# Kernel optimization log

Measured on AMD Instinct MI355X. Metric: run time of the kernel, lower is better.

Reference implementation:

```python
import jax, jax.numpy as jnp
import numpy as np

B, SRC_LEN, IN_DIM = 4096, 128, 16
H = 64
SEQ_LEN = 100
MEAN_DIM = 4
COV_DIM = MEAN_DIM + MEAN_DIM * (MEAN_DIM - 1) // 2  # 10
SKIP = 4


def _lin_init(key, out_d, in_d):
    k1, k2 = jax.random.split(key)
    bound = 1.0 / np.sqrt(in_d)
    W = jax.random.uniform(k1, (out_d, in_d), minval=-bound, maxval=bound, dtype=jnp.float32)
    b = jax.random.uniform(k2, (out_d,), minval=-bound, maxval=bound, dtype=jnp.float32)
    return W, b


def setup_inputs() -> dict:
    key = jax.random.key(0)
    ks = jax.random.split(key, 16)
    inp = {}
    inp["x"] = jax.random.normal(ks[0], (B, SRC_LEN, IN_DIM), dtype=jnp.float32)
    inp["trg"] = jax.random.normal(ks[1], (B, 1, SKIP), dtype=jnp.float32)
    # encoder GRU (1 layer)
    inp["enc_Wih"], inp["enc_bih"] = _lin_init(ks[2], 3 * H, IN_DIM)
    inp["enc_Whh"], inp["enc_bhh"] = _lin_init(ks[3], 3 * H, H)
    # decoder GRU (1 layer)
    inp["dec_Wih"], inp["dec_bih"] = _lin_init(ks[4], 3 * H, IN_DIM)
    inp["dec_Whh"], inp["dec_bhh"] = _lin_init(ks[5], 3 * H, H)
    # decoder.out: Linear(H -> IN_DIM)
    inp["out_W"], inp["out_b"] = _lin_init(ks[6], IN_DIM, H)
    # initEmbed: Linear(SKIP -> IN_DIM)
    inp["emb_W"], inp["emb_b"] = _lin_init(ks[7], IN_DIM, SKIP)
    # mean head: Linear(IN_DIM->H), GELU, Linear(H->MEAN_DIM)
    inp["mh_W1"], inp["mh_b1"] = _lin_init(ks[8], H, IN_DIM)
    inp["mh_W2"], inp["mh_b2"] = _lin_init(ks[9], MEAN_DIM, H)
    # cov head: Linear(IN_DIM->H), GELU, Linear(H->COV_DIM)
    inp["ch_W1"], inp["ch_b1"] = _lin_init(ks[10], H, IN_DIM)
    inp["ch_W2"], inp["ch_b2"] = _lin_init(ks[11], COV_DIM, H)
    return inp


def _gru_cell(h, xt, Wih, Whh, bih, bhh):
    # PyTorch GRU cell math. h, xt: [B, H], [B, in]
    gi = xt @ Wih.T + bih           # [B, 3H]
    gh = h @ Whh.T + bhh            # [B, 3H]
    i_r, i_z, i_n = jnp.split(gi, 3, axis=-1)
    h_r, h_z, h_n = jnp.split(gh, 3, axis=-1)
    r = jax.nn.sigmoid(i_r + h_r)
    z = jax.nn.sigmoid(i_z + h_z)
    n = jnp.tanh(i_n + r * h_n)
    return (1.0 - z) * n + z * h


def reference(x, trg, enc_Wih, enc_bih, enc_Whh, enc_bhh,
              dec_Wih, dec_bih, dec_Whh, dec_bhh,
              out_W, out_b, emb_W, emb_b,
              mh_W1, mh_b1, mh_W2, mh_b2,
              ch_W1, ch_b1, ch_W2, ch_b2):
    b = x.shape[0]
    # ---- encoder GRU over src_len; only final hidden is used downstream ----
    h0 = jnp.zeros((b, H), dtype=x.dtype)

    def enc_step(h, xt):
        h = _gru_cell(h, xt, enc_Wih, enc_Whh, enc_bih, enc_bhh)
        return h, None

    enc_h, _ = jax.lax.scan(enc_step, h0, jnp.swapaxes(x, 0, 1))

    init_in = trg[:, 0, :] @ emb_W.T + emb_b  # [B, IN_DIM]

    def dec_step(carry, _):
        h, inp = carry
        h = _gru_cell(h, inp, dec_Wih, dec_Whh, dec_bih, dec_bhh)
        o = h @ out_W.T + out_b               # [B, IN_DIM]
        nxt = jax.lax.stop_gradient(o)        # .detach() on fed-back input
        return (h, nxt), o

    (_, _), outs = jax.lax.scan(dec_step, (enc_h, init_in), None, length=SEQ_LEN)
    dec_out = jnp.swapaxes(outs, 0, 1)        # [B, SEQ_LEN, IN_DIM]

    # ---- output heads (Dropout is identity in eval) ----
    means = jax.nn.gelu(dec_out @ mh_W1.T + mh_b1, approximate=False) @ mh_W2.T + mh_b2
    covs = jax.nn.gelu(dec_out @ ch_W1.T + ch_b1, approximate=False) @ ch_W2.T + ch_b2

    inf = jnp.inf
    lower = jnp.array([-inf, -inf, -1.0, -1.0], dtype=means.dtype)
    upper = jnp.array([inf, inf, 1.0, 1.0], dtype=means.dtype)
    means = jnp.maximum(jnp.minimum(means, upper), lower)
    return means, covs
```

## Files before the change

### kernel.cpp

```cpp
#include <hip/hip_runtime.h>
#include <cstdint>
#include <cstddef>

#define BTOT    4096
#define SRCLEN  128
#define INDIM   16
#define HDIM    64
#define SEQLEN  100
#define MEANS_N (BTOT * SEQLEN * 4)

__device__ __forceinline__ float sigmoidf_(float x) {
    return __builtin_amdgcn_rcpf(1.0f + __expf(-x));
}
__device__ __forceinline__ float tanhf_(float x) {
    float e = __expf(2.0f * x);
    return 1.0f - 2.0f * __builtin_amdgcn_rcpf(e + 1.0f);
}
__device__ __forceinline__ float gelu_fast(float x) {
    float z = fabsf(x) * 0.70710678118654752440f;
    float t = __builtin_amdgcn_rcpf(1.0f + 0.3275911f * z);
    float p = t * (0.254829592f +
              t * (-0.284496736f +
              t * (1.421413741f +
              t * (-1.453152027f +
              t * 1.061405429f))));
    float er = 1.0f - p * __expf(-z * z);
    er = copysignf(er, x);
    return 0.5f * x * (1.0f + er);
}

typedef __attribute__((ext_vector_type(8))) short s8v;
typedef __attribute__((ext_vector_type(4))) float f4v;

__device__ __forceinline__ unsigned short f2bf(float x) {
    unsigned u = __float_as_uint(x);
    unsigned r = (u + 0x7FFFu + ((u >> 16) & 1u)) >> 16;
    return (unsigned short)r;
}
__device__ __forceinline__ float bf2f(unsigned short b) {
    return __uint_as_float(((unsigned)b) << 16);
}
__device__ __forceinline__ void split2(float4 a, float4 b, s8v& hi, s8v& lo) {
    float v[8] = {a.x, a.y, a.z, a.w, b.x, b.y, b.z, b.w};
    #pragma unroll
    for (int j = 0; j < 8; ++j) {
        unsigned short h = f2bf(v[j]);
        hi[j] = (short)h;
        lo[j] = (short)f2bf(v[j] - bf2f(h));
    }
}
__device__ __forceinline__ void split8(const float* v, s8v& hi, s8v& lo) {
    #pragma unroll
    for (int j = 0; j < 8; ++j) {
        unsigned short h = f2bf(v[j]);
        hi[j] = (short)h;
        lo[j] = (short)f2bf(v[j] - bf2f(h));
    }
}
__device__ __forceinline__ void load_bfrag(const float* p, s8v& hi, s8v& lo) {
    float4 a = *(const float4*)p;
    float4 b = *(const float4*)(p + 4);
    split2(a, b, hi, lo);
}

typedef __attribute__((ext_vector_type(2))) unsigned int u2v;
__device__ __forceinline__ float half_merge(float own_lo, float send_hi) {
    u2v r = __builtin_amdgcn_permlane32_swap(__float_as_uint(own_lo),
                                             __float_as_uint(send_hi),
                                             false, false);
    return __uint_as_float(r[0]);
}

#define MFMA16(a, b, c) __builtin_amdgcn_mfma_f32_16x16x32_bf16((a), (b), (c), 0, 0, 0)

__global__ __launch_bounds__(256, 2) void fused_gru_kernel(
    const float* __restrict__ x,
    const float* __restrict__ eWih, const float* __restrict__ ebih,
    const float* __restrict__ eWhh, const float* __restrict__ ebhh,
    const float* __restrict__ dWih, const float* __restrict__ dbih,
    const float* __restrict__ dWhh, const float* __restrict__ dbhh,
    const float* __restrict__ outW, const float* __restrict__ outb,
    const float* __restrict__ embW, const float* __restrict__ embb,
    const float* __restrict__ trg,
    float* __restrict__ dec_o)
{
    const int tid  = threadIdx.x;
    const int lane = tid & 63;
    const int w    = tid >> 6;
    const int col  = lane & 15;
    const int q    = lane >> 4;
    const int u    = w * 16 + col;
    const int b0   = blockIdx.x * 8;
    const int rj0  = (q & 1) * 4 + ((q >> 1) << 1);

    __shared__ __align__(16) unsigned short hiL[2][16][72];
    __shared__ __align__(16) unsigned short loL[2][16][72];
    __shared__ __align__(16) unsigned short xhi_l[64][9][16];
    __shared__ __align__(16) unsigned short xlo_l[64][9][16];
    __shared__ float outW_l[16][64];
    __shared__ float init_l[8][16];

    for (int i = tid; i < 16 * 64; i += 256) outW_l[i >> 6][i & 63] = outW[i];
    if (tid < 128) {
        int b = tid >> 4, jj = tid & 15;
        float s = embb[jj];
        #pragma unroll
        for (int s4 = 0; s4 < 4; ++s4)
            s = fmaf(embW[jj * 4 + s4], trg[(size_t)(b0 + b) * 4 + s4], s);
        init_l[b][jj] = s;
    }

    for (int i = tid; i < 2 * 16 * 72; i += 256) {
        ((unsigned short*)hiL)[i] = 0;
        ((unsigned short*)loL)[i] = 0;
    }
    for (int i = tid; i < 64 * 16; i += 256) {
        xhi_l[i >> 4][8][i & 15] = 0;
        xlo_l[i >> 4][8][i & 15] = 0;
    }

    auto stage_x = [&](int c) {
        #pragma unroll
        for (int k = 0; k < 8; ++k) {
            int f   = tid + k * 256;
            int b   = f >> 8;
            int rem = f & 255;
            int tl  = rem >> 2;
            int d4  = (rem & 3) << 2;
            const float* xp = x + ((size_t)(b0 + b) * SRCLEN + (c * 64 + tl)) * INDIM + d4;
            float4 v = *(const float4*)xp;
            float vv[4] = {v.x, v.y, v.z, v.w};
            unsigned short hh[4], ll[4];
            #pragma unroll
            for (int j = 0; j < 4; ++j) {
                hh[j] = f2bf(vv[j]);
                ll[j] = f2bf(vv[j] - bf2f(hh[j]));
            }
            *(ushort4*)&xhi_l[tl][b][d4] = make_ushort4(hh[0], hh[1], hh[2], hh[3]);
            *(ushort4*)&xlo_l[tl][b][d4] = make_ushort4(ll[0], ll[1], ll[2], ll[3]);
        }
    };

    const s8v z8 = {0, 0, 0, 0, 0, 0, 0, 0};
    const f4v z4 = {0.0f, 0.0f, 0.0f, 0.0f};

    {
        s8v brh[3], brl[3], bzh[3], bzl[3], bnhh[2], bnhl[2], bnxh, bnxl;
        load_bfrag(eWhh + (size_t)u * 64 + q * 8,              brh[0], brl[0]);
        load_bfrag(eWhh + (size_t)u * 64 + 32 + q * 8,         brh[1], brl[1]);
        load_bfrag(eWhh + (size_t)(64 + u) * 64 + q * 8,       bzh[0], bzl[0]);
        load_bfrag(eWhh + (size_t)(64 + u) * 64 + 32 + q * 8,  bzh[1], bzl[1]);
        load_bfrag(eWhh + (size_t)(128 + u) * 64 + q * 8,      bnhh[0], bnhl[0]);
        load_bfrag(eWhh + (size_t)(128 + u) * 64 + 32 + q * 8, bnhh[1], bnhl[1]);
        if (q < 2) {
            load_bfrag(eWih + (size_t)u * 16 + q * 8,         brh[2], brl[2]);
            load_bfrag(eWih + (size_t)(64 + u) * 16 + q * 8,  bzh[2], bzl[2]);
            load_bfrag(eWih + (size_t)(128 + u) * 16 + q * 8, bnxh, bnxl);
        } else {
            brh[2] = z8; brl[2] = z8; bzh[2] = z8; bzl[2] = z8; bnxh = z8; bnxl = z8;
        }

        const float br   = ebih[u] + ebhh[u];
        const float bz   = ebih[u + 64] + ebhh[u + 64];
        const float bnx  = ebih[u + 128];
        const float bnh  = ebhh[u + 128];

        const int xb   = (q < 2) ? (col & 7) : 8;
        const int xoff = (q & 1) * 8;
        const unsigned short* xh_base = &xhi_l[0][xb][xoff];
        const unsigned short* xl_base = &xlo_l[0][xb][xoff];

        stage_x(0);
        float hold2e[2] = {0.0f, 0.0f};
        __syncthreads();

        int cur = 0;
        for (int t = 0; t < SRCLEN; ++t) {
            if (t == 64) {
                stage_x(1);
                __syncthreads();
            }
            const int tl = t & 63;

            const s8v xh = *(const s8v*)(xh_base + (size_t)tl * 144);
            const s8v xl = *(const s8v*)(xl_base + (size_t)tl * 144);

            const s8v ah0 = *(const s8v*)&hiL[cur][col][q * 8];
            const s8v al0 = *(const s8v*)&loL[cur][col][q * 8];
            const s8v ah1 = *(const s8v*)&hiL[cur][col][32 + q * 8];
            const s8v al1 = *(const s8v*)&loL[cur][col][32 + q * 8];

            f4v accr, accz, accnh, accnx;
            accr  = MFMA16(ah0, brh[0], z4);
            accz  = MFMA16(ah0, bzh[0], z4);
            accnh = MFMA16(ah0, bnhh[0], z4);
            accr  = MFMA16(ah0, brl[0], accr);
            accz  = MFMA16(ah0, bzl[0], accz);
            accnh = MFMA16(ah0, bnhl[0], accnh);
            accr  = MFMA16(al0, brh[0], accr);
            accz  = MFMA16(al0, bzh[0], accz);
            accnh = MFMA16(al0, bnhh[0], accnh);
            accr  = MFMA16(ah1, brh[1], accr);
            accz  = MFMA16(ah1, bzh[1], accz);
            accnh = MFMA16(ah1, bnhh[1], accnh);
            accr  = MFMA16(ah1, brl[1], accr);
            accz  = MFMA16(ah1, bzl[1], accz);
            accnh = MFMA16(ah1, bnhl[1], accnh);
            accr  = MFMA16(al1, brh[1], accr);
            accz  = MFMA16(al1, bzh[1], accz);
            accnh = MFMA16(al1, bnhh[1], accnh);
            accr  = MFMA16(xh, brh[2], accr);
            accz  = MFMA16(xh, bzh[2], accz);
            accnx = MFMA16(xh, bnxh, z4);
            accr  = MFMA16(xh, brl[2], accr);
            accz  = MFMA16(xh, bzl[2], accz);
            accnx = MFMA16(xh, bnxl, accnx);
            accr  = MFMA16(xl, brh[2], accr);
            accz  = MFMA16(xl, bzh[2], accz);
            accnx = MFMA16(xl, bnxh, accnx);

            float pr[2], pz[2], pnh[2], pnx[2];
            pr[0]  = half_merge(accr[0],  accr[2]);
            pr[1]  = half_merge(accr[1],  accr[3]);
            pz[0]  = half_merge(accz[0],  accz[2]);
            pz[1]  = half_merge(accz[1],  accz[3]);
            pnh[0] = half_merge(accnh[0], accnh[2]);
            pnh[1] = half_merge(accnh[1], accnh[3]);
            pnx[0] = half_merge(accnx[0], accnx[2]);
            pnx[1] = half_merge(accnx[1], accnx[3]);

            const int nxt = cur ^ 1;
            #pragma unroll
            for (int j = 0; j < 2; ++j) {
                float r  = sigmoidf_(pr[j] + br);
                float zz = sigmoidf_(pz[j] + bz);
                float n  = tanhf_(pnx[j] + bnx + r * (pnh[j] + bnh));
                float h  = (1.0f - zz) * n + zz * hold2e[j];
                hold2e[j] = h;
                unsigned short hh = f2bf(h);
                hiL[nxt][rj0 + j][u] = hh;
                loL[nxt][rj0 + j][u] = f2bf(h - bf2f(hh));
            }
            __syncthreads();
            cur ^= 1;
        }

        float hold2[2] = {hold2e[0], hold2e[1]};

        float wh_r[16], wh_z[16], wh_n[16];
        #pragma unroll
        for (int c = 0; c < 2; ++c)
            #pragma unroll
            for (int jj = 0; jj < 8; ++jj) {
                int k = c * 32 + q * 8 + jj;
                wh_r[c * 8 + jj] = dWhh[(size_t)u * 64 + k];
                wh_z[c * 8 + jj] = dWhh[(size_t)(64 + u) * 64 + k];
                wh_n[c * 8 + jj] = dWhh[(size_t)(128 + u) * 64 + k];
            }
        float wi_r[16], wi_z[16], wi_n[16];
        #pragma unroll
        for (int j = 0; j < 16; ++j) {
            wi_r[j] = dWih[(size_t)u * 16 + j];
            wi_z[j] = dWih[(size_t)(64 + u) * 16 + j];
            wi_n[j] = dWih[(size_t)(128 + u) * 16 + j];
        }

        float m_r[16], m_z[16], c_in[16];
        #pragma unroll
        for (int c = 0; c < 2; ++c)
            #pragma unroll
            for (int jj = 0; jj < 8; ++jj) {
                int k = c * 32 + q * 8 + jj;
                float sr = 0.0f, sz = 0.0f, sn = 0.0f;
                #pragma unroll
                for (int j = 0; j < 16; ++j) {
                    float ow = outW_l[j][k];
                    sr = fmaf(wi_r[j], ow, sr);
                    sz = fmaf(wi_z[j], ow, sz);
                    sn = fmaf(wi_n[j], ow, sn);
                }
                m_r[c * 8 + jj]  = wh_r[c * 8 + jj] + sr;
                m_z[c * 8 + jj]  = wh_z[c * 8 + jj] + sz;
                c_in[c * 8 + jj] = sn;
            }

        s8v mrh[2], mrl[2], mzh[2], mzl[2], cinh[2], cinl[2], hnh[2], hnl[2];
        split8(m_r,      mrh[0],  mrl[0]);  split8(m_r + 8,  mrh[1],  mrl[1]);
        split8(m_z,      mzh[0],  mzl[0]);  split8(m_z + 8,  mzh[1],  mzl[1]);
        split8(c_in,     cinh[0], cinl[0]); split8(c_in + 8, cinh[1], cinl[1]);
        split8(wh_n,     hnh[0],  hnl[0]);  split8(wh_n + 8, hnh[1],  hnl[1]);
        s8v r0h[2], r0l[2], z0h[2], z0l[2];
        split8(wh_r, r0h[0], r0l[0]); split8(wh_r + 8, r0h[1], r0l[1]);
        split8(wh_z, z0h[0], z0l[0]); split8(wh_z + 8, z0h[1], z0l[1]);
        s8v owh[2], owl[2];
        {
            float ov[16];
            #pragma unroll
            for (int c = 0; c < 2; ++c)
                #pragma unroll
                for (int jj = 0; jj < 8; ++jj)
                    ov[c * 8 + jj] = outW_l[col][c * 32 + q * 8 + jj];
            split8(ov, owh[0], owl[0]); split8(ov + 8, owh[1], owl[1]);
        }

        float b_r = dbhh[u] + dbih[u];
        float b_z = dbhh[u + 64] + dbih[u + 64];
        float b_in = dbih[u + 128];
        const float b_hn = dbhh[u + 128];
        #pragma unroll
        for (int j = 0; j < 16; ++j) {
            float obj = outb[j];
            b_r  = fmaf(obj, wi_r[j], b_r);
            b_z  = fmaf(obj, wi_z[j], b_z);
            b_in = fmaf(obj, wi_n[j], b_in);
        }
        const float ob = outb[col];

        float g_r[2], g_z[2], g_n[2];
        #pragma unroll
        for (int j2 = 0; j2 < 2; ++j2) {
            int row = rj0 + j2;
            float sr = dbih[u] + dbhh[u];
            float sz = dbih[u + 64] + dbhh[u + 64];
            float sn = dbih[u + 128];
            #pragma unroll
            for (int j = 0; j < 16; ++j) {
                float iv = init_l[row][j];
                sr = fmaf(wi_r[j], iv, sr);
                sz = fmaf(wi_z[j], iv, sz);
                sn = fmaf(wi_n[j], iv, sn);
            }
            g_r[j2] = sr; g_z[j2] = sz; g_n[j2] = sn;
        }

        {
            const s8v ah0 = *(const s8v*)&hiL[0][col][q * 8];
            const s8v al0 = *(const s8v*)&loL[0][col][q * 8];
            const s8v ah1 = *(const s8v*)&hiL[0][col][32 + q * 8];
            const s8v al1 = *(const s8v*)&loL[0][col][32 + q * 8];
            f4v ar, az, ahn;
            ar  = MFMA16(ah0, r0h[0], z4);
            az  = MFMA16(ah0, z0h[0], z4);
            ahn = MFMA16(ah0, hnh[0], z4);
            ar  = MFMA16(ah0, r0l[0], ar);
            az  = MFMA16(ah0, z0l[0], az);
            ahn = MFMA16(ah0, hnl[0], ahn);
            ar  = MFMA16(al0, r0h[0], ar);
            az  = MFMA16(al0, z0h[0], az);
            ahn = MFMA16(al0, hnh[0], ahn);
            ar  = MFMA16(ah1, r0h[1], ar);
            az  = MFMA16(ah1, z0h[1], az);
            ahn = MFMA16(ah1, hnh[1], ahn);
            ar  = MFMA16(ah1, r0l[1], ar);
            az  = MFMA16(ah1, z0l[1], az);
            ahn = MFMA16(ah1, hnl[1], ahn);
            ar  = MFMA16(al1, r0h[1], ar);
            az  = MFMA16(al1, z0h[1], az);
            ahn = MFMA16(al1, hnh[1], ahn);

            float pr[2], pz[2], pnh[2];
            pr[0]  = half_merge(ar[0],  ar[2]);
            pr[1]  = half_merge(ar[1],  ar[3]);
            pz[0]  = half_merge(az[0],  az[2]);
            pz[1]  = half_merge(az[1],  az[3]);
            pnh[0] = half_merge(ahn[0], ahn[2]);
            pnh[1] = half_merge(ahn[1], ahn[3]);

            #pragma unroll
            for (int j = 0; j < 2; ++j) {
                float r  = sigmoidf_(pr[j] + g_r[j]);
                float zz = sigmoidf_(pz[j] + g_z[j]);
                float n  = tanhf_(g_n[j] + r * (pnh[j] + b_hn));
                float h  = (1.0f - zz) * n + zz * hold2[j];
                hold2[j] = h;
                unsigned short hh = f2bf(h);
                hiL[1][rj0 + j][u] = hh;
                loL[1][rj0 + j][u] = f2bf(h - bf2f(hh));
            }
            __syncthreads();
        }

        for (int t = 1; t < SEQLEN; ++t) {
            const int dcur = t & 1;
            const s8v ah0 = *(const s8v*)&hiL[dcur][col][q * 8];
            const s8v al0 = *(const s8v*)&loL[dcur][col][q * 8];
            const s8v ah1 = *(const s8v*)&hiL[dcur][col][32 + q * 8];
            const s8v al1 = *(const s8v*)&loL[dcur][col][32 + q * 8];

            if (w == ((t - 1) & 3)) {
                f4v oa;
                oa = MFMA16(ah0, owh[0], z4);
                oa = MFMA16(ah0, owl[0], oa);
                oa = MFMA16(al0, owh[0], oa);
                oa = MFMA16(ah1, owh[1], oa);
                oa = MFMA16(ah1, owl[1], oa);
                oa = MFMA16(al1, owh[1], oa);
                if (q < 2) {
                    #pragma unroll
                    for (int i = 0; i < 4; ++i)
                        dec_o[(((size_t)(b0 + q * 4 + i) * SEQLEN) + (t - 1)) * INDIM + col] = oa[i] + ob;
                }
            }

            f4v ar, az, ain, ahn;
            ar  = MFMA16(ah0, mrh[0], z4);
            az  = MFMA16(ah0, mzh[0], z4);
            ain = MFMA16(ah0, cinh[0], z4);
            ahn = MFMA16(ah0, hnh[0], z4);
            ar  = MFMA16(ah0, mrl[0], ar);
            az  = MFMA16(ah0, mzl[0], az);
            ain = MFMA16(ah0, cinl[0], ain);
            ahn = MFMA16(ah0, hnl[0], ahn);
            ar  = MFMA16(al0, mrh[0], ar);
            az  = MFMA16(al0, mzh[0], az);
            ain = MFMA16(al0, cinh[0], ain);
            ahn = MFMA16(al0, hnh[0], ahn);
            ar  = MFMA16(ah1, mrh[1], ar);
            az  = MFMA16(ah1, mzh[1], az);
            ain = MFMA16(ah1, cinh[1], ain);
            ahn = MFMA16(ah1, hnh[1], ahn);
            ar  = MFMA16(ah1, mrl[1], ar);
            az  = MFMA16(ah1, mzl[1], az);
            ain = MFMA16(ah1, cinl[1], ain);
            ahn = MFMA16(ah1, hnl[1], ahn);
            ar  = MFMA16(al1, mrh[1], ar);
            az  = MFMA16(al1, mzh[1], az);
            ain = MFMA16(al1, cinh[1], ain);
            ahn = MFMA16(al1, hnh[1], ahn);

            float pr[2], pz[2], pin[2], pnh[2];
            pr[0]  = half_merge(ar[0],  ar[2]);
            pr[1]  = half_merge(ar[1],  ar[3]);
            pz[0]  = half_merge(az[0],  az[2]);
            pz[1]  = half_merge(az[1],  az[3]);
            pin[0] = half_merge(ain[0], ain[2]);
            pin[1] = half_merge(ain[1], ain[3]);
            pnh[0] = half_merge(ahn[0], ahn[2]);
            pnh[1] = half_merge(ahn[1], ahn[3]);

            const int nxt = dcur ^ 1;
            #pragma unroll
            for (int j = 0; j < 2; ++j) {
                float r  = sigmoidf_(pr[j] + b_r);
                float zz = sigmoidf_(pz[j] + b_z);
                float n  = tanhf_(pin[j] + b_in + r * (pnh[j] + b_hn));
                float h  = (1.0f - zz) * n + zz * hold2[j];
                hold2[j] = h;
                unsigned short hh = f2bf(h);
                hiL[nxt][rj0 + j][u] = hh;
                loL[nxt][rj0 + j][u] = f2bf(h - bf2f(hh));
            }
            __syncthreads();
        }

        if (w == 0) {
            const s8v ah0 = *(const s8v*)&hiL[0][col][q * 8];
            const s8v al0 = *(const s8v*)&loL[0][col][q * 8];
            const s8v ah1 = *(const s8v*)&hiL[0][col][32 + q * 8];
            const s8v al1 = *(const s8v*)&loL[0][col][32 + q * 8];
            f4v oa;
            oa = MFMA16(ah0, owh[0], z4);
            oa = MFMA16(ah0, owl[0], oa);
            oa = MFMA16(al0, owh[0], oa);
            oa = MFMA16(ah1, owh[1], oa);
            oa = MFMA16(ah1, owl[1], oa);
            oa = MFMA16(al1, owh[1], oa);
            if (q < 2) {
                #pragma unroll
                for (int i = 0; i < 4; ++i)
                    dec_o[(((size_t)(b0 + q * 4 + i) * SEQLEN) + (SEQLEN - 1)) * INDIM + col] = oa[i] + ob;
            }
        }
    }
}

__global__ __launch_bounds__(256) void heads_kernel(
    const float* __restrict__ dec_o,
    const float* __restrict__ mW1, const float* __restrict__ mb1,
    const float* __restrict__ mW2, const float* __restrict__ mb2,
    const float* __restrict__ cW1, const float* __restrict__ cb1,
    const float* __restrict__ cW2, const float* __restrict__ cb2,
    float* __restrict__ out)
{
    const int tid = threadIdx.x;

    __shared__ __align__(16) float lW1m[64][16];
    __shared__ __align__(16) float lW1c[64][16];
    __shared__ __align__(16) float lW2t[64][16];

    for (int i = tid; i < 1024; i += 256) {
        lW1m[i >> 4][i & 15] = mW1[i];
        lW1c[i >> 4][i & 15] = cW1[i];
    }
    if (tid < 64) {
        #pragma unroll
        for (int j = 0; j < 4; ++j)  lW2t[tid][j]     = mW2[j * 64 + tid];
        #pragma unroll
        for (int j = 0; j < 10; ++j) lW2t[tid][4 + j] = cW2[j * 64 + tid];
        lW2t[tid][14] = mb1[tid];
        lW2t[tid][15] = cb1[tid];
    }
    __syncthreads();

    const size_t r0 = (size_t)blockIdx.x * 512 + tid;

    float o[2][16];
    #pragma unroll
    for (int k = 0; k < 2; ++k) {
        const float4* op = (const float4*)(dec_o + (r0 + (size_t)k * 256) * 16);
        #pragma unroll
        for (int c = 0; c < 4; ++c) {
            float4 v = op[c];
            o[k][4 * c + 0] = v.x; o[k][4 * c + 1] = v.y;
            o[k][4 * c + 2] = v.z; o[k][4 * c + 3] = v.w;
        }
    }

    float m[2][4], cv[2][10];
    #pragma unroll
    for (int k = 0; k < 2; ++k) {
        #pragma unroll
        for (int j = 0; j < 4; ++j)  m[k][j]  = mb2[j];
        #pragma unroll
        for (int j = 0; j < 10; ++j) cv[k][j] = cb2[j];
    }

    #pragma unroll 2
    for (int hu = 0; hu < 64; ++hu) {
        const float4 a0 = *(const float4*)&lW1m[hu][0];
        const float4 a1 = *(const float4*)&lW1m[hu][4];
        const float4 a2 = *(const float4*)&lW1m[hu][8];
        const float4 a3 = *(const float4*)&lW1m[hu][12];
        const float4 c0 = *(const float4*)&lW1c[hu][0];
        const float4 c1 = *(const float4*)&lW1c[hu][4];
        const float4 c2 = *(const float4*)&lW1c[hu][8];
        const float4 c3 = *(const float4*)&lW1c[hu][12];
        const float4 t0 = *(const float4*)&lW2t[hu][0];
        const float4 t1 = *(const float4*)&lW2t[hu][4];
        const float4 t2 = *(const float4*)&lW2t[hu][8];
        const float4 t3 = *(const float4*)&lW2t[hu][12];

        #pragma unroll
        for (int k = 0; k < 2; ++k) {
            float hm = t3.z;
            hm = fmaf(a0.x, o[k][0],  hm); hm = fmaf(a0.y, o[k][1],  hm);
            hm = fmaf(a0.z, o[k][2],  hm); hm = fmaf(a0.w, o[k][3],  hm);
            hm = fmaf(a1.x, o[k][4],  hm); hm = fmaf(a1.y, o[k][5],  hm);
            hm = fmaf(a1.z, o[k][6],  hm); hm = fmaf(a1.w, o[k][7],  hm);
            hm = fmaf(a2.x, o[k][8],  hm); hm = fmaf(a2.y, o[k][9],  hm);
            hm = fmaf(a2.z, o[k][10], hm); hm = fmaf(a2.w, o[k][11], hm);
            hm = fmaf(a3.x, o[k][12], hm); hm = fmaf(a3.y, o[k][13], hm);
            hm = fmaf(a3.z, o[k][14], hm); hm = fmaf(a3.w, o[k][15], hm);
            float gm = gelu_fast(hm);
            m[k][0] = fmaf(t0.x, gm, m[k][0]); m[k][1] = fmaf(t0.y, gm, m[k][1]);
            m[k][2] = fmaf(t0.z, gm, m[k][2]); m[k][3] = fmaf(t0.w, gm, m[k][3]);

            float hc = t3.w;
            hc = fmaf(c0.x, o[k][0],  hc); hc = fmaf(c0.y, o[k][1],  hc);
            hc = fmaf(c0.z, o[k][2],  hc); hc = fmaf(c0.w, o[k][3],  hc);
            hc = fmaf(c1.x, o[k][4],  hc); hc = fmaf(c1.y, o[k][5],  hc);
            hc = fmaf(c1.z, o[k][6],  hc); hc = fmaf(c1.w, o[k][7],  hc);
            hc = fmaf(c2.x, o[k][8],  hc); hc = fmaf(c2.y, o[k][9],  hc);
            hc = fmaf(c2.z, o[k][10], hc); hc = fmaf(c2.w, o[k][11], hc);
            hc = fmaf(c3.x, o[k][12], hc); hc = fmaf(c3.y, o[k][13], hc);
            hc = fmaf(c3.z, o[k][14], hc); hc = fmaf(c3.w, o[k][15], hc);
            float gc = gelu_fast(hc);
            cv[k][0] = fmaf(t1.x, gc, cv[k][0]); cv[k][1] = fmaf(t1.y, gc, cv[k][1]);
            cv[k][2] = fmaf(t1.z, gc, cv[k][2]); cv[k][3] = fmaf(t1.w, gc, cv[k][3]);
            cv[k][4] = fmaf(t2.x, gc, cv[k][4]); cv[k][5] = fmaf(t2.y, gc, cv[k][5]);
            cv[k][6] = fmaf(t2.z, gc, cv[k][6]); cv[k][7] = fmaf(t2.w, gc, cv[k][7]);
            cv[k][8] = fmaf(t3.x, gc, cv[k][8]); cv[k][9] = fmaf(t3.y, gc, cv[k][9]);
        }
    }

    float* means = out;
    float* covs  = out + MEANS_N;
    #pragma unroll
    for (int k = 0; k < 2; ++k) {
        const size_t r = r0 + (size_t)k * 256;
        m[k][2] = fminf(fmaxf(m[k][2], -1.0f), 1.0f);
        m[k][3] = fminf(fmaxf(m[k][3], -1.0f), 1.0f);
        #pragma unroll
        for (int j = 0; j < 4; ++j)  means[r * 4 + j] = m[k][j];
        #pragma unroll
        for (int j = 0; j < 10; ++j) covs[r * 10 + j] = cv[k][j];
    }
}

extern "C" void kernel_launch(void* const* d_in, const int* in_sizes, int n_in,
                              void* d_out, int out_size, void* d_ws, size_t ws_size,
                              hipStream_t stream)
{
    const float* x    = (const float*)d_in[0];
    const float* trg  = (const float*)d_in[1];
    const float* eWih = (const float*)d_in[2];
    const float* ebih = (const float*)d_in[3];
    const float* eWhh = (const float*)d_in[4];
    const float* ebhh = (const float*)d_in[5];
    const float* dWih = (const float*)d_in[6];
    const float* dbih = (const float*)d_in[7];
    const float* dWhh = (const float*)d_in[8];
    const float* dbhh = (const float*)d_in[9];
    const float* outW = (const float*)d_in[10];
    const float* outb = (const float*)d_in[11];
    const float* embW = (const float*)d_in[12];
    const float* embb = (const float*)d_in[13];
    const float* mW1  = (const float*)d_in[14];
    const float* mb1  = (const float*)d_in[15];
    const float* mW2  = (const float*)d_in[16];
    const float* mb2  = (const float*)d_in[17];
    const float* cW1  = (const float*)d_in[18];
    const float* cb1  = (const float*)d_in[19];
    const float* cW2  = (const float*)d_in[20];
    const float* cb2  = (const float*)d_in[21];

    float* ws    = (float*)d_ws;
    float* dec_o = ws;
    float* outp  = (float*)d_out;

    fused_gru_kernel<<<dim3(BTOT / 8), dim3(256), 0, stream>>>(
        x, eWih, ebih, eWhh, ebhh, dWih, dbih, dWhh, dbhh,
        outW, outb, embW, embb, trg, dec_o);
    heads_kernel<<<dim3((BTOT * SEQLEN) / 512), dim3(256), 0, stream>>>(
        dec_o, mW1, mb1, mW2, mb2, cW1, cb1, cW2, cb2, outp);
}
```

Measured before the change: 358.4 us.

## Rewrite output heads kernel with split-bf16 MFMA matmuls

Replaces the scalar FMA head MLP with a per-wave MFMA formulation. Both linear layers of the mean and cov heads use bf16 hi/lo split products (three MFMAs per product) to keep near-fp32 accuracy. The GELU hidden activations are staged through LDS as bf16 hi/lo pairs. Each wave handles four 16-row tiles. This aims to cut the VALU-bound FMA cost of the heads, but adds LDS traffic and stores only partially utilized MFMA output columns.

```diff
diff --git a/kernel.cpp b/kernel.cpp
--- a/kernel.cpp
+++ b/kernel.cpp
@@ -474,7 +474,7 @@
     }
 }
 
-__global__ __launch_bounds__(256) void heads_kernel(
+__global__ __launch_bounds__(256) void heads_mfma_kernel(
     const float* __restrict__ dec_o,
     const float* __restrict__ mW1, const float* __restrict__ mb1,
     const float* __restrict__ mW2, const float* __restrict__ mb2,
@@ -482,108 +482,125 @@
     const float* __restrict__ cW2, const float* __restrict__ cb2,
     float* __restrict__ out)
 {
-    const int tid = threadIdx.x;
-
-    __shared__ __align__(16) float lW1m[64][16];
-    __shared__ __align__(16) float lW1c[64][16];
-    __shared__ __align__(16) float lW2t[64][16];
-
-    for (int i = tid; i < 1024; i += 256) {
-        lW1m[i >> 4][i & 15] = mW1[i];
-        lW1c[i >> 4][i & 15] = cW1[i];
-    }
-    if (tid < 64) {
-        #pragma unroll
-        for (int j = 0; j < 4; ++j)  lW2t[tid][j]     = mW2[j * 64 + tid];
-        #pragma unroll
-        for (int j = 0; j < 10; ++j) lW2t[tid][4 + j] = cW2[j * 64 + tid];
-        lW2t[tid][14] = mb1[tid];
-        lW2t[tid][15] = cb1[tid];
-    }
-    __syncthreads();
-
-    const size_t r0 = (size_t)blockIdx.x * 512 + tid;
-
-    float o[2][16];
+    const int tid  = threadIdx.x;
+    const int lane = tid & 63;
+    const int w    = tid >> 6;
+    const int col  = lane & 15;
+    const int q    = lane >> 4;
+
+    __shared__ __align__(16) unsigned short Hm_hi[4][16][72];
+    __shared__ __align__(16) unsigned short Hm_lo[4][16][72];
+    __shared__ __align__(16) unsigned short Hc_hi[4][16][72];
+    __shared__ __align__(16) unsigned short Hc_lo[4][16][72];
+
+    const s8v z8 = {0, 0, 0, 0, 0, 0, 0, 0};
+    const f4v z4 = {0.0f, 0.0f, 0.0f, 0.0f};
+
+    s8v w1mh[4], w1ml[4], w1ch[4], w1cl[4];
     #pragma unroll
-    for (int k = 0; k < 2; ++k) {
-        const float4* op = (const float4*)(dec_o + (r0 + (size_t)k * 256) * 16);
-        #pragma unroll
-        for (int c = 0; c < 4; ++c) {
-            float4 v = op[c];
-            o[k][4 * c + 0] = v.x; o[k][4 * c + 1] = v.y;
-            o[k][4 * c + 2] = v.z; o[k][4 * c + 3] = v.w;
-        }
-    }
-
-    float m[2][4], cv[2][10];
+    for (int c = 0; c < 4; ++c) {
+        if (q < 2) {
+            load_bfrag(mW1 + (size_t)(c * 16 + col) * 16 + q * 8, w1mh[c], w1ml[c]);
+            load_bfrag(cW1 + (size_t)(c * 16 + col) * 16 + q * 8, w1ch[c], w1cl[c]);
+        } else {
+            w1mh[c] = z8; w1ml[c] = z8; w1ch[c] = z8; w1cl[c] = z8;
+        }
+    }
+    s8v w2mh[2], w2ml[2], w2ch[2], w2cl[2];
+    if (col < 4) {
+        load_bfrag(mW2 + (size_t)col * 64 + q * 8,      w2mh[0], w2ml[0]);
+        load_bfrag(mW2 + (size_t)col * 64 + 32 + q * 8, w2mh[1], w2ml[1]);
+    } else {
+        w2mh[0] = z8; w2ml[0] = z8; w2mh[1] = z8; w2ml[1] = z8;
+    }
+    if (col < 10) {
+        load_bfrag(cW2 + (size_t)col * 64 + q * 8,      w2ch[0], w2cl[0]);
+        load_bfrag(cW2 + (size_t)col * 64 + 32 + q * 8, w2ch[1], w2cl[1]);
+    } else {
+        w2ch[0] = z8; w2cl[0] = z8; w2ch[1] = z8; w2cl[1] = z8;
+    }
+
+    float b1m[4], b1c[4];
     #pragma unroll
-    for (int k = 0; k < 2; ++k) {
-        #pragma unroll
-        for (int j = 0; j < 4; ++j)  m[k][j]  = mb2[j];
-        #pragma unroll
-        for (int j = 0; j < 10; ++j) cv[k][j] = cb2[j];
-    }
-
-    #pragma unroll 2
-    for (int hu = 0; hu < 64; ++hu) {
-        const float4 a0 = *(const float4*)&lW1m[hu][0];
-        const float4 a1 = *(const float4*)&lW1m[hu][4];
-        const float4 a2 = *(const float4*)&lW1m[hu][8];
-        const float4 a3 = *(const float4*)&lW1m[hu][12];
-        const float4 c0 = *(const float4*)&lW1c[hu][0];
-        const float4 c1 = *(const float4*)&lW1c[hu][4];
-        const float4 c2 = *(const float4*)&lW1c[hu][8];
-        const float4 c3 = *(const float4*)&lW1c[hu][12];
-        const float4 t0 = *(const float4*)&lW2t[hu][0];
-        const float4 t1 = *(const float4*)&lW2t[hu][4];
-        const float4 t2 = *(const float4*)&lW2t[hu][8];
-        const float4 t3 = *(const float4*)&lW2t[hu][12];
-
-        #pragma unroll
-        for (int k = 0; k < 2; ++k) {
-            float hm = t3.z;
-            hm = fmaf(a0.x, o[k][0],  hm); hm = fmaf(a0.y, o[k][1],  hm);
-            hm = fmaf(a0.z, o[k][2],  hm); hm = fmaf(a0.w, o[k][3],  hm);
-            hm = fmaf(a1.x, o[k][4],  hm); hm = fmaf(a1.y, o[k][5],  hm);
-            hm = fmaf(a1.z, o[k][6],  hm); hm = fmaf(a1.w, o[k][7],  hm);
-            hm = fmaf(a2.x, o[k][8],  hm); hm = fmaf(a2.y, o[k][9],  hm);
-            hm = fmaf(a2.z, o[k][10], hm); hm = fmaf(a2.w, o[k][11], hm);
-            hm = fmaf(a3.x, o[k][12], hm); hm = fmaf(a3.y, o[k][13], hm);
-            hm = fmaf(a3.z, o[k][14], hm); hm = fmaf(a3.w, o[k][15], hm);
-            float gm = gelu_fast(hm);
-            m[k][0] = fmaf(t0.x, gm, m[k][0]); m[k][1] = fmaf(t0.y, gm, m[k][1]);
-            m[k][2] = fmaf(t0.z, gm, m[k][2]); m[k][3] = fmaf(t0.w, gm, m[k][3]);
-
-            float hc = t3.w;
-            hc = fmaf(c0.x, o[k][0],  hc); hc = fmaf(c0.y, o[k][1],  hc);
-            hc = fmaf(c0.z, o[k][2],  hc); hc = fmaf(c0.w, o[k][3],  hc);
-            hc = fmaf(c1.x, o[k][4],  hc); hc = fmaf(c1.y, o[k][5],  hc);
-            hc = fmaf(c1.z, o[k][6],  hc); hc = fmaf(c1.w, o[k][7],  hc);
-            hc = fmaf(c2.x, o[k][8],  hc); hc = fmaf(c2.y, o[k][9],  hc);
-            hc = fmaf(c2.z, o[k][10], hc); hc = fmaf(c2.w, o[k][11], hc);
-            hc = fmaf(c3.x, o[k][12], hc); hc = fmaf(c3.y, o[k][13], hc);
-            hc = fmaf(c3.z, o[k][14], hc); hc = fmaf(c3.w, o[k][15], hc);
-            float gc = gelu_fast(hc);
-            cv[k][0] = fmaf(t1.x, gc, cv[k][0]); cv[k][1] = fmaf(t1.y, gc, cv[k][1]);
-            cv[k][2] = fmaf(t1.z, gc, cv[k][2]); cv[k][3] = fmaf(t1.w, gc, cv[k][3]);
-            cv[k][4] = fmaf(t2.x, gc, cv[k][4]); cv[k][5] = fmaf(t2.y, gc, cv[k][5]);
-            cv[k][6] = fmaf(t2.z, gc, cv[k][6]); cv[k][7] = fmaf(t2.w, gc, cv[k][7]);
-            cv[k][8] = fmaf(t3.x, gc, cv[k][8]); cv[k][9] = fmaf(t3.y, gc, cv[k][9]);
-        }
-    }
+    for (int c = 0; c < 4; ++c) {
+        b1m[c] = mb1[c * 16 + col];
+        b1c[c] = cb1[c * 16 + col];
+    }
+    const float b2m = (col < 4)  ? mb2[col] : 0.0f;
+    const float b2c = (col < 10) ? cb2[col] : 0.0f;
 
     float* means = out;
     float* covs  = out + MEANS_N;
-    #pragma unroll
-    for (int k = 0; k < 2; ++k) {
-        const size_t r = r0 + (size_t)k * 256;
-        m[k][2] = fminf(fmaxf(m[k][2], -1.0f), 1.0f);
-        m[k][3] = fminf(fmaxf(m[k][3], -1.0f), 1.0f);
-        #pragma unroll
-        for (int j = 0; j < 4; ++j)  means[r * 4 + j] = m[k][j];
-        #pragma unroll
-        for (int j = 0; j < 10; ++j) covs[r * 10 + j] = cv[k][j];
+
+    const int wave_id = blockIdx.x * 4 + w;
+
+    #pragma unroll 1
+    for (int it = 0; it < 4; ++it) {
+        const int tile = wave_id + 6400 * it;
+        const size_t r0 = (size_t)tile * 16;
+
+        s8v ah, al;
+        if (q < 2) {
+            load_bfrag(dec_o + (r0 + (size_t)col) * 16 + q * 8, ah, al);
+        } else { ah = z8; al = z8; }
+
+        #pragma unroll
+        for (int c = 0; c < 4; ++c) {
+            f4v am = MFMA16(ah, w1mh[c], z4);
+            am = MFMA16(ah, w1ml[c], am);
+            am = MFMA16(al, w1mh[c], am);
+            f4v ac = MFMA16(ah, w1ch[c], z4);
+            ac = MFMA16(ah, w1cl[c], ac);
+            ac = MFMA16(al, w1ch[c], ac);
+            #pragma unroll
+            for (int i = 0; i < 4; ++i) {
+                float hm = gelu_fast(am[i] + b1m[c]);
+                unsigned short hh = f2bf(hm);
+                Hm_hi[w][q * 4 + i][c * 16 + col] = hh;
+                Hm_lo[w][q * 4 + i][c * 16 + col] = f2bf(hm - bf2f(hh));
+                float hc = gelu_fast(ac[i] + b1c[c]);
+                hh = f2bf(hc);
+                Hc_hi[w][q * 4 + i][c * 16 + col] = hh;
+                Hc_lo[w][q * 4 + i][c * 16 + col] = f2bf(hc - bf2f(hh));
+            }
+        }
+
+        const s8v amh0 = *(const s8v*)&Hm_hi[w][col][q * 8];
+        const s8v amh1 = *(const s8v*)&Hm_hi[w][col][32 + q * 8];
+        const s8v aml0 = *(const s8v*)&Hm_lo[w][col][q * 8];
+        const s8v aml1 = *(const s8v*)&Hm_lo[w][col][32 + q * 8];
+        const s8v ach0 = *(const s8v*)&Hc_hi[w][col][q * 8];
+        const s8v ach1 = *(const s8v*)&Hc_hi[w][col][32 + q * 8];
+        const s8v acl0 = *(const s8v*)&Hc_lo[w][col][q * 8];
+        const s8v acl1 = *(const s8v*)&Hc_lo[w][col][32 + q * 8];
+
+        f4v om, oc;
+        om = MFMA16(amh0, w2mh[0], z4);
+        om = MFMA16(amh0, w2ml[0], om);
+        om = MFMA16(aml0, w2mh[0], om);
+        om = MFMA16(amh1, w2mh[1], om);
+        om = MFMA16(amh1, w2ml[1], om);
+        om = MFMA16(aml1, w2mh[1], om);
+        oc = MFMA16(ach0, w2ch[0], z4);
+        oc = MFMA16(ach0, w2cl[0], oc);
+        oc = MFMA16(acl0, w2ch[0], oc);
+        oc = MFMA16(ach1, w2ch[1], oc);
+        oc = MFMA16(ach1, w2cl[1], oc);
+        oc = MFMA16(acl1, w2ch[1], oc);
+
+        if (col < 4) {
+            #pragma unroll
+            for (int i = 0; i < 4; ++i) {
+                float v = om[i] + b2m;
+                if (col >= 2) v = fminf(fmaxf(v, -1.0f), 1.0f);
+                means[(r0 + q * 4 + i) * 4 + col] = v;
+            }
+        }
+        if (col < 10) {
+            #pragma unroll
+            for (int i = 0; i < 4; ++i)
+                covs[(r0 + q * 4 + i) * 10 + col] = oc[i] + b2c;
+        }
     }
 }
 
@@ -621,6 +638,6 @@
     fused_gru_kernel<<<dim3(BTOT / 8), dim3(256), 0, stream>>>(
         x, eWih, ebih, eWhh, ebhh, dWih, dbih, dWhh, dbhh,
         outW, outb, embW, embb, trg, dec_o);
-    heads_kernel<<<dim3((BTOT * SEQLEN) / 512), dim3(256), 0, stream>>>(
+    heads_mfma_kernel<<<dim3(1600), dim3(256), 0, stream>>>(
         dec_o, mW1, mb1, mW2, mb2, cW1, cb1, cW2, cb2, outp);
 }
```

Result: faster. 349.0 us (-2.6%).
